# Performance work log

Measured on AMD Instinct MI355X. Metric: run time of the kernel, lower is better.

The kernel has to match this reference:

```python
import jax, jax.numpy as jnp
import numpy as np

HEAD_SIZE = 64


def setup_inputs() -> dict:
    key = jax.random.key(0)
    k1, k2, k3, k4 = jax.random.split(key, 4)
    x = jax.random.normal(k1, (4, 4096, 1024), dtype=jnp.float32)
    Wk = jax.random.normal(k2, (1024, HEAD_SIZE), dtype=jnp.float32) * 0.02
    Wq = jax.random.normal(k3, (1024, HEAD_SIZE), dtype=jnp.float32) * 0.02
    Wv = jax.random.normal(k4, (1024, HEAD_SIZE), dtype=jnp.float32) * 0.02
    return {"x": x, "Wk": Wk, "Wq": Wq, "Wv": Wv}


def reference(x, Wk, Wq, Wv):
    # x: [B, S, D]; projections (Linear without bias): x @ W -> [B, S, H]
    k = jnp.einsum('bsd,dh->bsh', x, Wk)
    q = jnp.einsum('bsd,dh->bsh', x, Wq)
    v = jnp.einsum('bsd,dh->bsh', x, Wv)
    scale = 1.0 / np.sqrt(HEAD_SIZE).astype(np.float32)
    z = jnp.einsum('bqh,bkh->bqk', q, k) * scale  # [B, S, S]
    S = x.shape[1]
    causal = jnp.tril(jnp.ones((S, S), dtype=bool))
    z = jnp.where(causal, z, -jnp.inf)
    z = jax.nn.softmax(z, axis=2)
    return jnp.einsum('bqk,bkh->bqh', z, v)
```

## Files before the change

kernel.cpp:

```cpp
#include <hip/hip_runtime.h>
#include <hip/hip_bf16.h>
#include <stdint.h>
#include <math.h>

typedef __attribute__((ext_vector_type(8))) short short8;
typedef __attribute__((ext_vector_type(4))) short short4v;
typedef __attribute__((ext_vector_type(4))) float float4v;

#define MFMA16(a,b,c) __builtin_amdgcn_mfma_f32_16x16x32_bf16((a),(b),(c),0,0,0)

__device__ __forceinline__ short bf16r(float f) {
  union { float f; uint32_t u; } v; v.f = f;
  uint32_t r = v.u + 0x7fffu + ((v.u >> 16) & 1u);
  return (short)(r >> 16);
}
__device__ __forceinline__ float bf2f(short s) {
  union { float f; uint32_t u; } v; v.u = ((uint32_t)(uint16_t)s) << 16;
  return v.f;
}
__device__ __forceinline__ uint32_t cvtpk(float a, float b) {
  uint32_t r;
  asm("v_cvt_pk_bf16_f32 %0, %1, %2" : "=v"(r) : "v"(a), "v"(b));
  return r;
}

__device__ __forceinline__ void gld_lds16(void* lds, const void* g) {
  __builtin_amdgcn_global_load_lds(
      (const __attribute__((address_space(1))) uint32_t*)g,
      (__attribute__((address_space(3))) uint32_t*)lds, 16, 0, 0);
}

__global__ __launch_bounds__(256) void prep_wt(
    const float* __restrict__ Wk, const float* __restrict__ Wq,
    const float* __restrict__ Wv, short* __restrict__ WT) {
  __shared__ float tile[64][65];
  const int w = blockIdx.y;
  const int k0 = blockIdx.x * 64;
  const float* W = (w == 0) ? Wk : (w == 1) ? Wq : Wv;
  const int tid = threadIdx.x;
#pragma unroll
  for (int i = 0; i < 16; ++i) {
    int e = i * 256 + tid;
    int kk = e >> 6, hh = e & 63;
    tile[kk][hh] = W[(size_t)(k0 + kk) * 64 + hh];
  }
  __syncthreads();
#pragma unroll
  for (int i = 0; i < 16; ++i) {
    int e = i * 256 + tid;
    int hh = e >> 6, kk = e & 63;
    WT[(size_t)w * 65536 + hh * 1024 + k0 + kk] = bf16r(tile[kk][hh]);
  }
}

__global__ __launch_bounds__(512, 4) void proj_kernel(
    const float* __restrict__ x, const short* __restrict__ WT,
    short* __restrict__ Kg, short* __restrict__ Qg, short* __restrict__ Vt) {
  __shared__ __align__(16) short xs[2][32][72];
  __shared__ __align__(16) short wts[2][192 * 64];
  const int tid = threadIdx.x;
  const int lane = tid & 63;
  const int w = tid >> 6;
  const int c = lane & 15;
  const int sl = lane >> 4;
  const int mh = w & 1;
  const int nh = w >> 1;
  const int m0 = blockIdx.x * 32;

  float4v acc[3];
#pragma unroll
  for (int ni = 0; ni < 3; ++ni) acc[ni] = (float4v){0.f, 0.f, 0.f, 0.f};

  const int srow = tid >> 4;
  const int scol = (tid & 15) * 4;
  const float* xrow = x + (size_t)(m0 + srow) * 1024 + scol;

#define PSTAGE_WT(buf, kk)                                                    \
  _Pragma("unroll") for (int rr = 0; rr < 3; ++rr) {                          \
    const int chunk = rr * 512 + tid;                                         \
    const int n = chunk >> 3;                                                 \
    const int cc = chunk & 7;                                                 \
    gld_lds16(wts[buf] + chunk * 8,                                           \
              WT + (size_t)n * 1024 + (kk) + ((cc ^ (n & 7)) * 8));           \
  }
#define PWRITE_X(buf)                                                         \
  {                                                                           \
    short4v hx;                                                               \
    hx.x = bf16r(xr.x); hx.y = bf16r(xr.y);                                   \
    hx.z = bf16r(xr.z); hx.w = bf16r(xr.w);                                   \
    *(short4v*)(&xs[buf][srow][scol]) = hx;                                   \
  }

  float4v xr = *(const float4v*)(xrow);
  float4v xn = *(const float4v*)(xrow + 64);

  PSTAGE_WT(0, 0)
  PWRITE_X(0)
  __syncthreads();

  int cur = 0;
  for (int it = 0; it < 16; ++it) {
    const int k0 = it * 64;
    if (it + 1 < 16) {
      PSTAGE_WT(cur ^ 1, k0 + 64)
      xr = xn;
      PWRITE_X(cur ^ 1)
      if (it + 2 < 16) xn = *(const float4v*)(xrow + k0 + 128);
    }
    short8 a0 = *(const short8*)(&xs[cur][mh * 16 + c][sl * 8]);
    short8 a1 = *(const short8*)(&xs[cur][mh * 16 + c][32 + sl * 8]);
#pragma unroll
    for (int ni = 0; ni < 3; ++ni) {
      const int rw = (nh * 3 + ni) * 16 + c;
      short8 b0 = *(const short8*)(wts[cur] + rw * 64 + ((sl ^ (rw & 7)) * 8));
      short8 b1 = *(const short8*)(wts[cur] + rw * 64 + (((sl + 4) ^ (rw & 7)) * 8));
      acc[ni] = MFMA16(a0, b0, acc[ni]);
      acc[ni] = MFMA16(a1, b1, acc[ni]);
    }
    __syncthreads();
    cur ^= 1;
  }
#undef PSTAGE_WT
#undef PWRITE_X

  const int b = m0 >> 12;
  const int s_base = m0 & 4095;
  const float QSCALE = 0.18033688011112042f;
#pragma unroll
  for (int ni = 0; ni < 3; ++ni) {
    const int nt = nh * 3 + ni;
    const int wsel = nt >> 2;
    const int h = (nt & 3) * 16 + c;
    const int q_local = mh * 16 + sl * 4;
    if (wsel == 2) {
      short4v pv;
      pv.x = bf16r(acc[ni].x); pv.y = bf16r(acc[ni].y);
      pv.z = bf16r(acc[ni].z); pv.w = bf16r(acc[ni].w);
      *(short4v*)(Vt + (size_t)(b * 64 + h) * 4096 + s_base + q_local) = pv;
    } else if (wsel == 1) {
#pragma unroll
      for (int i = 0; i < 4; ++i)
        Qg[(size_t)(m0 + q_local + i) * 64 + h] = bf16r(acc[ni][i] * QSCALE);
    } else {
#pragma unroll
      for (int i = 0; i < 4; ++i)
        Kg[(size_t)(m0 + q_local + i) * 64 + h] = bf16r(acc[ni][i]);
    }
  }
}

#define SLOT_BYTES 16896
__global__ __launch_bounds__(512, 4) void attn_kernel(
    const short* __restrict__ Qg, const short* __restrict__ Kg,
    const short* __restrict__ Vt, float* __restrict__ out,
    char* __restrict__ part, int split) {
  __shared__ __align__(16) short Ks[2][64 * 64];
  __shared__ __align__(16) short Vs[2][64 * 64];
  const int tid = threadIdx.x;
  const int lane = tid & 63;
  const int w = tid >> 6;
  const int c = lane & 15;
  const int sl = lane >> 4;

  int g, ch, b, uu = 0;
  if (split) {
    const int lin = (blockIdx.x & 7) * 136 + (blockIdx.x >> 3);
    b = lin / 272;
    uu = lin - b * 272;
    g = (int)(2.0f * sqrtf((float)uu));
    while (((g + 2) >> 1) * ((g + 3) >> 1) <= uu) ++g;
    while (((g + 1) >> 1) * ((g + 2) >> 1) > uu) --g;
    ch = uu - ((g + 1) >> 1) * ((g + 2) >> 1);
  } else { g = blockIdx.x; b = blockIdx.y; ch = 0; }
  const int T = 2 * (g + 1);
  const int c0 = ch * 4;
  const int c1 = (!split || c0 + 4 > T) ? T : c0 + 4;
  const int nch = split ? ((g >> 1) + 1) : 1;
  const int qw = g * 128 + w * 16;

  const short* Kb = Kg + (size_t)b * 4096 * 64;
  const short* Vb = Vt + (size_t)b * 64 * 4096;

  short8 aq0, aq1;
  {
    const short* qp = Qg + (size_t)(b * 4096 + qw + c) * 64 + sl * 8;
    aq0 = *(const short8*)(qp);
    aq1 = *(const short8*)(qp + 32);
  }

  float4v o[4];
#pragma unroll
  for (int ht = 0; ht < 4; ++ht) o[ht] = (float4v){0.f, 0.f, 0.f, 0.f};
  float lsum = 0.f;

#define STAGE(buf, t)                                                        \
  {                                                                          \
    const int kv0s = (t) * 64;                                               \
    const int rw = tid >> 3;                                                 \
    const int scol = ((tid & 7) ^ (rw & 7)) * 8;                             \
    gld_lds16(Ks[buf] + tid * 8, Kb + (size_t)(kv0s + rw) * 64 + scol);      \
    gld_lds16(Vs[buf] + tid * 8, Vb + (size_t)rw * 4096 + kv0s + scol);      \
  }

  STAGE(0, c0)
  __syncthreads();

  const int srcA = c + 32 * (sl & 1);
  const int srcB = srcA + 16;

  int cur = 0;
  for (int t = c0; t < c1; ++t) {
    const int kv0 = t * 64;
    if (t + 1 < c1) STAGE(cur ^ 1, t + 1)

    const short* KsC = Ks[cur];
    const short* VsC = Vs[cur];

    float4v s[4];
    __builtin_amdgcn_s_setprio(1);
#pragma unroll
    for (int nt = 0; nt < 4; ++nt) {
      const int rw = nt * 16 + c;
      short8 kb0 = *(const short8*)(KsC + rw * 64 + ((sl ^ (rw & 7)) * 8));
      short8 kb1 = *(const short8*)(KsC + rw * 64 + (((sl + 4) ^ (rw & 7)) * 8));
      float4v z = {0.f, 0.f, 0.f, 0.f};
      z = MFMA16(kb0, aq0, z);
      z = MFMA16(kb1, aq1, z);
      s[nt] = z;
    }
    __builtin_amdgcn_s_setprio(0);

    if (kv0 + 63 > qw) {
      const int qg = qw + c;
#pragma unroll
      for (int nt = 0; nt < 4; ++nt)
#pragma unroll
        for (int i = 0; i < 4; ++i) {
          const int kvg = kv0 + nt * 16 + sl * 4 + i;
          s[nt][i] = (kvg <= qg) ? s[nt][i] : -1e30f;
        }
    }

    uint32_t tpk[4][2];
#pragma unroll
    for (int nt = 0; nt < 4; ++nt) {
      const float p0 = exp2f(s[nt][0]);
      const float p1 = exp2f(s[nt][1]);
      const float p2 = exp2f(s[nt][2]);
      const float p3 = exp2f(s[nt][3]);
      lsum += (p0 + p1) + (p2 + p3);
      tpk[nt][0] = cvtpk(p0, p1);
      tpk[nt][1] = cvtpk(p2, p3);
    }

    short8 ap[2];
#pragma unroll
    for (int f = 0; f < 2; ++f) {
      const uint32_t q0a = __shfl((int)tpk[2 * f][0], srcA);
      const uint32_t q0b = __shfl((int)tpk[2 * f + 1][0], srcA);
      const uint32_t q1a = __shfl((int)tpk[2 * f][1], srcA);
      const uint32_t q1b = __shfl((int)tpk[2 * f + 1][1], srcA);
      const uint32_t q2a = __shfl((int)tpk[2 * f][0], srcB);
      const uint32_t q2b = __shfl((int)tpk[2 * f + 1][0], srcB);
      const uint32_t q3a = __shfl((int)tpk[2 * f][1], srcB);
      const uint32_t q3b = __shfl((int)tpk[2 * f + 1][1], srcB);
      const bool lo = (sl < 2);
      union { uint32_t u[4]; short8 s8; } ua;
      ua.u[0] = lo ? q0a : q0b;
      ua.u[1] = lo ? q1a : q1b;
      ua.u[2] = lo ? q2a : q2b;
      ua.u[3] = lo ? q3a : q3b;
      ap[f] = ua.s8;
    }

    __builtin_amdgcn_s_setprio(1);
#pragma unroll
    for (int ht = 0; ht < 4; ++ht) {
      const int rw = ht * 16 + c;
      short8 vb0 = *(const short8*)(VsC + rw * 64 + ((sl ^ (rw & 7)) * 8));
      short8 vb1 = *(const short8*)(VsC + rw * 64 + (((sl + 4) ^ (rw & 7)) * 8));
      o[ht] = MFMA16(ap[0], vb0, o[ht]);
      o[ht] = MFMA16(ap[1], vb1, o[ht]);
    }
    __builtin_amdgcn_s_setprio(0);

    if (t + 1 < c1) __syncthreads();
    cur ^= 1;
  }
#undef STAGE

  float rsum = lsum;
  rsum += __shfl_xor(rsum, 16);
  rsum += __shfl_xor(rsum, 32);

  if (nch == 1) {
    float inv[4];
#pragma unroll
    for (int i = 0; i < 4; ++i)
      inv[i] = 1.0f / __shfl(rsum, sl * 4 + i);
#pragma unroll
    for (int ht = 0; ht < 4; ++ht)
#pragma unroll
      for (int i = 0; i < 4; ++i) {
        const int q = qw + sl * 4 + i;
        out[(size_t)(b * 4096 + q) * 64 + ht * 16 + c] = o[ht][i] * inv[i];
      }
  } else {
    short* sp = (short*)(part + (size_t)(b * 272 + uu) * SLOT_BYTES);
    float* lp = (float*)(sp + 8192);
#pragma unroll
    for (int ht = 0; ht < 4; ++ht)
#pragma unroll
      for (int i = 0; i < 4; ++i) {
        const int row = w * 16 + sl * 4 + i;
        sp[row * 64 + ht * 16 + c] = bf16r(o[ht][i]);
      }
    if (sl == 0) lp[w * 16 + c] = rsum;
  }
}

__global__ __launch_bounds__(256) void combine_kernel(
    const char* __restrict__ part, float* __restrict__ out) {
  const int g = blockIdx.x;
  const int b = blockIdx.y;
  const int N = (g >> 1) + 1;
  if (N == 1) return;
  const int F = ((g + 1) >> 1) * ((g + 2) >> 1);
  const char* base = part + (size_t)(b * 272 + F) * SLOT_BYTES;
  const int r = blockIdx.z * 32 + (threadIdx.x >> 3);
  const int cb = (threadIdx.x & 7) * 8;

  float L = 0.f;
  float acc[8];
#pragma unroll
  for (int k = 0; k < 8; ++k) acc[k] = 0.f;
  for (int i = 0; i < N; ++i) {
    const short* sp = (const short*)(base + (size_t)i * SLOT_BYTES);
    L += ((const float*)(sp + 8192))[r];
    short8 v = *(const short8*)(sp + r * 64 + cb);
#pragma unroll
    for (int j = 0; j < 8; ++j) acc[j] += bf2f(v[j]);
  }
  const float inv = 1.0f / L;
  float* op = out + (size_t)(b * 4096 + g * 128 + r) * 64 + cb;
  float4v r0 = {acc[0] * inv, acc[1] * inv, acc[2] * inv, acc[3] * inv};
  float4v r1 = {acc[4] * inv, acc[5] * inv, acc[6] * inv, acc[7] * inv};
  *(float4v*)(op) = r0;
  *(float4v*)(op + 4) = r1;
}

extern "C" void kernel_launch(void* const* d_in, const int* in_sizes, int n_in,
                              void* d_out, int out_size, void* d_ws, size_t ws_size,
                              hipStream_t stream) {
  const float* x  = (const float*)d_in[0];
  const float* Wk = (const float*)d_in[1];
  const float* Wq = (const float*)d_in[2];
  const float* Wv = (const float*)d_in[3];

  char* ws = (char*)d_ws;
  short* WT = (short*)ws;
  short* Kg = (short*)(ws + 393216);
  short* Qg = (short*)(ws + 393216 + 2097152);
  short* Vt = (short*)(ws + 393216 + 2 * 2097152);
  const size_t part_off = 393216 + 3 * 2097152;
  char* part = ws + part_off;

  const int split = (ws_size >= part_off + (size_t)1088 * SLOT_BYTES) ? 1 : 0;

  prep_wt<<<dim3(16, 3), dim3(256), 0, stream>>>(Wk, Wq, Wv, WT);
  proj_kernel<<<dim3(512), dim3(512), 0, stream>>>(x, WT, Kg, Qg, Vt);
  attn_kernel<<<split ? dim3(1088) : dim3(32, 4), dim3(512), 0, stream>>>(
      Qg, Kg, Vt, (float*)d_out, part, split);
  if (split)
    combine_kernel<<<dim3(32, 4, 4), dim3(256), 0, stream>>>(part, (float*)d_out);
}
```

Baseline: 61.05 us.

## Preload all chunk K/V tiles into LDS and drop per-tile barriers

After: 58.83 us. 1.04x faster.

```diff
diff --git a/kernel.cpp b/kernel.cpp
--- a/kernel.cpp
+++ b/kernel.cpp
@@ -154,8 +154,8 @@
     const short* __restrict__ Qg, const short* __restrict__ Kg,
     const short* __restrict__ Vt, float* __restrict__ out,
     char* __restrict__ part, int split) {
-  __shared__ __align__(16) short Ks[2][64 * 64];
-  __shared__ __align__(16) short Vs[2][64 * 64];
+  __shared__ __align__(16) short Ks[4][64 * 64];
+  __shared__ __align__(16) short Vs[4][64 * 64];
   const int tid = threadIdx.x;
   const int lane = tid & 63;
   const int w = tid >> 6;
@@ -176,6 +176,7 @@
   const int c0 = ch * 4;
   const int c1 = (!split || c0 + 4 > T) ? T : c0 + 4;
   const int nch = split ? ((g >> 1) + 1) : 1;
+  const int nt_loc = c1 - c0;
   const int qw = g * 128 + w * 16;
 
   const short* Kb = Kg + (size_t)b * 4096 * 64;
@@ -193,28 +194,27 @@
   for (int ht = 0; ht < 4; ++ht) o[ht] = (float4v){0.f, 0.f, 0.f, 0.f};
   float lsum = 0.f;
 
-#define STAGE(buf, t)                                                        \
-  {                                                                          \
-    const int kv0s = (t) * 64;                                               \
-    const int rw = tid >> 3;                                                 \
-    const int scol = ((tid & 7) ^ (rw & 7)) * 8;                             \
-    gld_lds16(Ks[buf] + tid * 8, Kb + (size_t)(kv0s + rw) * 64 + scol);      \
-    gld_lds16(Vs[buf] + tid * 8, Vb + (size_t)rw * 4096 + kv0s + scol);      \
-  }
-
-  STAGE(0, c0)
+  {
+    const int rw = tid >> 3;
+    const int scol = ((tid & 7) ^ (rw & 7)) * 8;
+#pragma unroll
+    for (int tt = 0; tt < 4; ++tt) {
+      if (tt < nt_loc) {
+        const int kv0s = (c0 + tt) * 64;
+        gld_lds16(Ks[tt] + tid * 8, Kb + (size_t)(kv0s + rw) * 64 + scol);
+        gld_lds16(Vs[tt] + tid * 8, Vb + (size_t)rw * 4096 + kv0s + scol);
+      }
+    }
+  }
   __syncthreads();
 
   const int srcA = c + 32 * (sl & 1);
   const int srcB = srcA + 16;
 
-  int cur = 0;
-  for (int t = c0; t < c1; ++t) {
-    const int kv0 = t * 64;
-    if (t + 1 < c1) STAGE(cur ^ 1, t + 1)
-
-    const short* KsC = Ks[cur];
-    const short* VsC = Vs[cur];
+  for (int tt = 0; tt < nt_loc; ++tt) {
+    const int kv0 = (c0 + tt) * 64;
+    const short* KsC = Ks[tt];
+    const short* VsC = Vs[tt];
 
     float4v s[4];
     __builtin_amdgcn_s_setprio(1);
@@ -283,11 +283,7 @@
       o[ht] = MFMA16(ap[1], vb1, o[ht]);
     }
     __builtin_amdgcn_s_setprio(0);
-
-    if (t + 1 < c1) __syncthreads();
-    cur ^= 1;
-  }
-#undef STAGE
+  }
 
   float rsum = lsum;
   rsum += __shfl_xor(rsum, 16);
```
